# Kernel tuning notes

Hardware: AMD Instinct MI355X
Metric: run time of the kernel (lower is better)

## Reference

```python
import jax, jax.numpy as jnp
import numpy as np

K = 1024
H = 16
HID = 4 * K
EPS = 1e-5


def _layernorm(x, g, b):
    mu = jnp.mean(x, axis=-1, keepdims=True)
    var = jnp.var(x, axis=-1, keepdims=True)
    return (x - mu) * jax.lax.rsqrt(var + EPS) * g + b


def _attention(xq, xkv, wq, wk, wv, wo, bo, causal):
    b, t, e = xq.shape
    tc = xkv.shape[1]
    h, s = H, e // H
    scale = e ** (-0.25)  # applied to both q and k, as in the original
    q = (xq @ wq).reshape(b, t, h, s) * scale
    k = (xkv @ wk).reshape(b, tc, h, s) * scale
    v = (xkv @ wv).reshape(b, tc, h, s)
    dot = jnp.einsum('bqhs,bkhs->bhqk', q, k)  # (b,h,t,tc)
    if causal:
        mask = jnp.tril(jnp.ones((t, tc), dtype=bool))
        dot = jnp.where(mask, dot, jnp.finfo(dot.dtype).min)
    att = jax.nn.softmax(dot, axis=-1)
    out = jnp.einsum('bhqk,bkhs->bqhs', att, v).reshape(b, t, e)
    return out @ wo + bo


def setup_inputs() -> dict:
    key = jax.random.key(0)
    ks = jax.random.split(key, 16)
    sd = K ** -0.5
    inp = {
        'x': jax.random.normal(ks[0], (4, 1024, K), jnp.float32),
        'context': jax.random.normal(ks[1], (4, 1024, K), jnp.float32),
        'sa_wq': jax.random.normal(ks[2], (K, K), jnp.float32) * sd,
        'sa_wk': jax.random.normal(ks[3], (K, K), jnp.float32) * sd,
        'sa_wv': jax.random.normal(ks[4], (K, K), jnp.float32) * sd,
        'sa_wo': jax.random.normal(ks[5], (K, K), jnp.float32) * sd,
        'sa_bo': jnp.zeros((K,), jnp.float32),
        'ca_wq': jax.random.normal(ks[6], (K, K), jnp.float32) * sd,
        'ca_wk': jax.random.normal(ks[7], (K, K), jnp.float32) * sd,
        'ca_wv': jax.random.normal(ks[8], (K, K), jnp.float32) * sd,
        'ca_wo': jax.random.normal(ks[9], (K, K), jnp.float32) * sd,
        'ca_bo': jnp.zeros((K,), jnp.float32),
        'n1_g': jnp.ones((K,), jnp.float32), 'n1_b': jnp.zeros((K,), jnp.float32),
        'n2_g': jnp.ones((K,), jnp.float32), 'n2_b': jnp.zeros((K,), jnp.float32),
        'n3_g': jnp.ones((K,), jnp.float32), 'n3_b': jnp.zeros((K,), jnp.float32),
        'ff_w1': jax.random.normal(ks[10], (K, HID), jnp.float32) * sd,
        'ff_b1': jnp.zeros((HID,), jnp.float32),
        'ff_w2': jax.random.normal(ks[11], (HID, K), jnp.float32) * (HID ** -0.5),
        'ff_b2': jnp.zeros((K,), jnp.float32),
    }
    return inp


def reference(x, context, sa_wq, sa_wk, sa_wv, sa_wo, sa_bo,
              ca_wq, ca_wk, ca_wv, ca_wo, ca_bo,
              n1_g, n1_b, n2_g, n2_b, n3_g, n3_b,
              ff_w1, ff_b1, ff_w2, ff_b2):
    # Masked self-attention + residual + LN (dropout is identity in eval mode)
    sa = _attention(x, x, sa_wq, sa_wk, sa_wv, sa_wo, sa_bo, causal=True)
    x = _layernorm(x + sa, n1_g, n1_b)
    # Cross-attention + residual + LN
    ca = _attention(x, context, ca_wq, ca_wk, ca_wv, ca_wo, ca_bo, causal=False)
    x = _layernorm(x + ca, n2_g, n2_b)
    # FFN + residual + LN
    ff = jax.nn.relu(x @ ff_w1 + ff_b1) @ ff_w2 + ff_b2
    x = _layernorm(x + ff, n3_g, n3_b)
    return x
```

## Files before the change

### kernel.cpp

```cpp
#include <hip/hip_runtime.h>

typedef __bf16 bf16x8 __attribute__((ext_vector_type(8)));
typedef __bf16 bf16x4 __attribute__((ext_vector_type(4)));
typedef float floatx4 __attribute__((ext_vector_type(4)));

#define EMB 1024
#define MROWS 4096
#define HIDN 4096
#define PSTRIDE ((size_t)MROWS * EMB)

__device__ __forceinline__ void load_lds16(const __bf16* g, __bf16* l) {
    __builtin_amdgcn_global_load_lds(
        (const __attribute__((address_space(1))) void*)g,
        (__attribute__((address_space(3))) void*)l, 16, 0, 0);
}

__global__ void transpose_cast_kernel(const float* __restrict__ in,
                                      __bf16* __restrict__ out, int R, int C) {
    __shared__ float tile[32][33];
    int tx = threadIdx.x, ty = threadIdx.y;
    int c0 = blockIdx.x * 32, r0 = blockIdx.y * 32;
#pragma unroll
    for (int i = 0; i < 32; i += 8)
        tile[ty + i][tx] = in[(size_t)(r0 + ty + i) * C + c0 + tx];
    __syncthreads();
#pragma unroll
    for (int i = 0; i < 32; i += 8)
        out[(size_t)(c0 + ty + i) * R + r0 + tx] = (__bf16)tile[tx][ty + i];
}

struct TC8 { const float* s[8]; __bf16* d[8]; };
__global__ void transpose_cast8_kernel(TC8 a) {
    __shared__ float tile[32][33];
    const float* in = a.s[blockIdx.z];
    __bf16* out = a.d[blockIdx.z];
    int tx = threadIdx.x, ty = threadIdx.y;
    int c0 = blockIdx.x * 32, r0 = blockIdx.y * 32;
#pragma unroll
    for (int i = 0; i < 32; i += 8)
        tile[ty + i][tx] = in[(size_t)(r0 + ty + i) * EMB + c0 + tx];
    __syncthreads();
#pragma unroll
    for (int i = 0; i < 32; i += 8)
        out[(size_t)(c0 + ty + i) * EMB + r0 + tx] = (__bf16)tile[tx][ty + i];
}

__global__ void transpose_v_kernel(const __bf16* __restrict__ in,
                                   __bf16* __restrict__ vt, int ld, int Tc) {
    __shared__ __bf16 tile[32][33];
    int tx = threadIdx.x, ty = threadIdx.y;
    int t0 = blockIdx.x * 32, s0 = blockIdx.y * 32;
    int bh = blockIdx.z, b = bh >> 4, h = bh & 15;
#pragma unroll
    for (int i = 0; i < 32; i += 8)
        tile[ty + i][tx] = in[(size_t)(b * Tc + t0 + ty + i) * ld + h * 64 + s0 + tx];
    __syncthreads();
#pragma unroll
    for (int i = 0; i < 32; i += 8)
        vt[((size_t)bh * 64 + s0 + ty + i) * Tc + t0 + tx] = tile[tx][ty + i];
}

__global__ void cast_bf16_kernel(const float* __restrict__ in,
                                 __bf16* __restrict__ out, int n) {
    int i = (blockIdx.x * 256 + threadIdx.x) * 4;
    if (i >= n) return;
    float4 v = *(const float4*)(in + i);
    bf16x4 o;
    o[0] = (__bf16)v.x; o[1] = (__bf16)v.y; o[2] = (__bf16)v.z; o[3] = (__bf16)v.w;
    *(bf16x4*)(out + i) = o;
}

template <int RELU>
__launch_bounds__(256, 4)
__global__ void gemm_bt(const __bf16* __restrict__ A, const __bf16* __restrict__ Bt,
                        __bf16* __restrict__ cb, __bf16* __restrict__ cbalt,
                        const float* __restrict__ bias,
                        int M, int N, int Kd, float scale0, float scale1,
                        int split, int fx, int fy) {
    __shared__ alignas(16) __bf16 As[128 * 32];
    __shared__ alignas(16) __bf16 Bs[128 * 32];
    int tid  = threadIdx.x;
    int wv   = tid >> 6, lane = tid & 63;

    int L   = blockIdx.x + gridDim.x * (blockIdx.y + gridDim.y * blockIdx.z);
    int xcd = L & 7, j = L >> 3;
    int ff  = fx * fy;
    int zw  = xcd / ff;
    int rr  = xcd % ff;
    int nxf = gridDim.x / fx;
    int bnw = (j % nxf) * fx + (rr % fx);
    int bmw = (j / nxf) * fy + (rr / fx);
    int bn  = bnw * 128, bm = bmw * 128;

    int wm   = (wv & 1) * 64, wn = (wv >> 1) * 64;
    int l16  = lane & 15, g16 = lane >> 4;

    int kc   = Kd / gridDim.z;
    int zoff = zw * kc;

    const __bf16* ag0 = A  + (size_t)(bm + (tid >> 2)) * Kd + zoff + (tid & 3) * 8;
    const __bf16* ag1 = ag0 + (size_t)64 * Kd;
    const __bf16* bg0 = Bt + (size_t)(bn + (tid >> 2)) * Kd + zoff + (tid & 3) * 8;
    const __bf16* bg1 = bg0 + (size_t)64 * Kd;
    __bf16* al0 = &As[tid * 8];
    __bf16* al1 = &As[2048 + tid * 8];
    __bf16* bl0 = &Bs[tid * 8];
    __bf16* bl1 = &Bs[2048 + tid * 8];

    floatx4 acc[4][4] = {};

    for (int k0 = 0; k0 < kc; k0 += 32) {
        __syncthreads();
        load_lds16(ag0, al0); load_lds16(ag1, al1);
        load_lds16(bg0, bl0); load_lds16(bg1, bl1);
        ag0 += 32; ag1 += 32; bg0 += 32; bg1 += 32;
        __syncthreads();
        bf16x8 af[4], bfr[4];
#pragma unroll
        for (int i = 0; i < 4; ++i)
            af[i] = *(const bf16x8*)&As[(wm + i * 16 + l16) * 32 + g16 * 8];
#pragma unroll
        for (int jj = 0; jj < 4; ++jj)
            bfr[jj] = *(const bf16x8*)&Bs[(wn + jj * 16 + l16) * 32 + g16 * 8];
#pragma unroll
        for (int i = 0; i < 4; ++i)
#pragma unroll
            for (int jj = 0; jj < 4; ++jj)
                acc[i][jj] = __builtin_amdgcn_mfma_f32_16x16x32_bf16(af[i], bfr[jj], acc[i][jj], 0, 0, 0);
    }

    __bf16* Cp = (zw == 0) ? cb : cbalt + (size_t)(zw - 1) * M * N;
    const float* bz = (zw == 0) ? bias : nullptr;

#pragma unroll
    for (int jj = 0; jj < 4; ++jj) {
        int col  = bn + wn + jj * 16 + l16;
        float sc = (col < split) ? scale0 : scale1;
        float bv = bz ? bz[col] : 0.f;
#pragma unroll
        for (int i = 0; i < 4; ++i) {
            int row0 = bm + wm + i * 16 + g16 * 4;
#pragma unroll
            for (int r = 0; r < 4; ++r) {
                float v = acc[i][jj][r] * sc + bv;
                if (RELU) v = fmaxf(v, 0.f);
                Cp[(size_t)(row0 + r) * N + col] = (__bf16)v;
            }
        }
    }
}

__launch_bounds__(256, 4)
__global__ void attn_kernel(const __bf16* __restrict__ qb, const __bf16* __restrict__ q2,
                            const __bf16* __restrict__ kb, const __bf16* __restrict__ vt,
                            int ldq, int ldk,
                            __bf16* __restrict__ out, int causal, int Tc) {
    constexpr int T = 1024;
    __shared__ alignas(16) __bf16 Qs[64 * 72];
    __shared__ alignas(16) __bf16 Ks[64 * 72];
    __shared__ alignas(16) __bf16 Vs[64 * 72];
    __shared__ alignas(16) __bf16 Ps[4][16 * 72];

    int tid = threadIdx.x;
    int wv = tid >> 6, lane = tid & 63;
    int qt = (blockIdx.x + 4 * blockIdx.z) & 15;
    int h = blockIdx.y, b = blockIdx.z;
    int l16 = lane & 15, g16 = lane >> 4;

#pragma unroll
    for (int cc = 0; cc < 2; ++cc) {
        int c = tid + cc * 256;
        int r = c >> 3, s8 = (c & 7) * 8;
        size_t go = (size_t)(b * T + qt * 64 + r) * ldq + h * 64 + s8;
        bf16x8 qv = *(const bf16x8*)(qb + go);
        if (q2) {
            bf16x8 q2v = *(const bf16x8*)(q2 + go);
#pragma unroll
            for (int e = 0; e < 8; ++e) qv[e] = (__bf16)((float)qv[e] + (float)q2v[e]);
        }
        *(bf16x8*)&Qs[r * 72 + s8] = qv;
    }

    floatx4 oacc[4] = {};
    float mi = -1e30f, li = 0.f;

    int ktmax = causal ? (qt + 1) : (Tc / 64);
    for (int kt = 0; kt < ktmax; ++kt) {
        __syncthreads();
#pragma unroll
        for (int cc = 0; cc < 2; ++cc) {
            int c = tid + cc * 256;
            int r = c >> 3, s8 = (c & 7) * 8;
            bf16x8 kv8 = *(const bf16x8*)(kb + (size_t)(b * Tc + kt * 64 + r) * ldk + h * 64 + s8);
            *(bf16x8*)&Ks[r * 72 + s8] = kv8;
            bf16x8 vv8 = *(const bf16x8*)(vt + ((size_t)(b * 16 + h) * 64 + r) * Tc + kt * 64 + s8);
            *(bf16x8*)&Vs[r * 72 + s8] = vv8;
        }
        __syncthreads();

        floatx4 sacc[4] = {};
#pragma unroll
        for (int kk = 0; kk < 2; ++kk) {
            bf16x8 bq = *(const bf16x8*)&Qs[(wv * 16 + l16) * 72 + kk * 32 + g16 * 8];
#pragma unroll
            for (int j = 0; j < 4; ++j) {
                bf16x8 ak = *(const bf16x8*)&Ks[(j * 16 + l16) * 72 + kk * 32 + g16 * 8];
                sacc[j] = __builtin_amdgcn_mfma_f32_16x16x32_bf16(ak, bq, sacc[j], 0, 0, 0);
            }
        }
        if (causal && kt == qt) {
            int qloc = wv * 16 + l16;
#pragma unroll
            for (int j = 0; j < 4; ++j)
#pragma unroll
                for (int r = 0; r < 4; ++r)
                    if (j * 16 + g16 * 4 + r > qloc) sacc[j][r] = -1e30f;
        }

        float mt = -1e30f;
#pragma unroll
        for (int j = 0; j < 4; ++j)
#pragma unroll
            for (int r = 0; r < 4; ++r) mt = fmaxf(mt, sacc[j][r]);
        mt = fmaxf(mt, __shfl_xor(mt, 16));
        mt = fmaxf(mt, __shfl_xor(mt, 32));
        float mnew  = fmaxf(mi, mt);
        float alpha = __expf(mi - mnew);
        mi = mnew;
        float ls = 0.f;
#pragma unroll
        for (int j = 0; j < 4; ++j) {
            bf16x4 pk;
#pragma unroll
            for (int r = 0; r < 4; ++r) {
                float p = __expf(sacc[j][r] - mnew);
                ls += p;
                pk[r] = (__bf16)p;
            }
            *(bf16x4*)&Ps[wv][l16 * 72 + j * 16 + g16 * 4] = pk;
        }
        ls += __shfl_xor(ls, 16);
        ls += __shfl_xor(ls, 32);
        li = li * alpha + ls;
#pragma unroll
        for (int j = 0; j < 4; ++j) {
            oacc[j][0] *= alpha; oacc[j][1] *= alpha;
            oacc[j][2] *= alpha; oacc[j][3] *= alpha;
        }
#pragma unroll
        for (int kk = 0; kk < 2; ++kk) {
            bf16x8 bp = *(const bf16x8*)&Ps[wv][l16 * 72 + kk * 32 + g16 * 8];
#pragma unroll
            for (int j = 0; j < 4; ++j) {
                bf16x8 av = *(const bf16x8*)&Vs[(j * 16 + l16) * 72 + kk * 32 + g16 * 8];
                oacc[j] = __builtin_amdgcn_mfma_f32_16x16x32_bf16(av, bp, oacc[j], 0, 0, 0);
            }
        }
    }

    __syncthreads();
    float inv = 1.f / li;
#pragma unroll
    for (int j = 0; j < 4; ++j) {
        bf16x4 ok;
#pragma unroll
        for (int r = 0; r < 4; ++r) ok[r] = (__bf16)(oacc[j][r] * inv);
        *(bf16x4*)&Ks[(wv * 16 + l16) * 72 + j * 16 + g16 * 4] = ok;
    }
    int rr = lane >> 2, c4 = (lane & 3) * 16;
    bf16x8 o0 = *(const bf16x8*)&Ks[(wv * 16 + rr) * 72 + c4];
    bf16x8 o1 = *(const bf16x8*)&Ks[(wv * 16 + rr) * 72 + c4 + 8];
    size_t ob = (size_t)(b * T + qt * 64 + wv * 16 + rr) * EMB + h * 64 + c4;
    *(bf16x8*)&out[ob]     = o0;
    *(bf16x8*)&out[ob + 8] = o1;
}

__launch_bounds__(256)
__global__ void ln_kernel(const float* __restrict__ res,
                          const __bf16* __restrict__ pb, int np,
                          const float* __restrict__ g, const float* __restrict__ be,
                          float* __restrict__ outf, __bf16* __restrict__ outb) {
    __shared__ float red[8];
    int row = blockIdx.x, tid = threadIdx.x;
    size_t base = (size_t)row * EMB;
    float4 v = ((const float4*)(res + base))[tid];
    for (int i = 0; i < np; ++i) {
        bf16x4 u = *(const bf16x4*)(pb + i * PSTRIDE + base + tid * 4);
        v.x += (float)u[0]; v.y += (float)u[1];
        v.z += (float)u[2]; v.w += (float)u[3];
    }
    float s  = v.x + v.y + v.z + v.w;
    float ss = v.x * v.x + v.y * v.y + v.z * v.z + v.w * v.w;
#pragma unroll
    for (int o = 1; o < 64; o <<= 1) { s += __shfl_xor(s, o); ss += __shfl_xor(ss, o); }
    if ((tid & 63) == 0) { red[(tid >> 6) * 2] = s; red[(tid >> 6) * 2 + 1] = ss; }
    __syncthreads();
    s  = red[0] + red[2] + red[4] + red[6];
    ss = red[1] + red[3] + red[5] + red[7];
    float mu  = s * (1.0f / 1024.0f);
    float var = ss * (1.0f / 1024.0f) - mu * mu;
    float rs  = rsqrtf(var + 1e-5f);
    float4 gg = ((const float4*)g)[tid];
    float4 bb = ((const float4*)be)[tid];
    float4 y;
    y.x = (v.x - mu) * rs * gg.x + bb.x;
    y.y = (v.y - mu) * rs * gg.y + bb.y;
    y.z = (v.z - mu) * rs * gg.z + bb.z;
    y.w = (v.w - mu) * rs * gg.w + bb.w;
    ((float4*)(outf + base))[tid] = y;
    if (outb) {
        bf16x4 o;
        o[0] = (__bf16)y.x; o[1] = (__bf16)y.y; o[2] = (__bf16)y.z; o[3] = (__bf16)y.w;
        *(bf16x4*)(outb + base + tid * 4) = o;
    }
}

extern "C" void kernel_launch(void* const* d_in, const int* in_sizes, int n_in,
                              void* d_out, int out_size, void* d_ws, size_t ws_size,
                              hipStream_t stream) {
    const float* x     = (const float*)d_in[0];
    const float* ctx   = (const float*)d_in[1];
    const float* sa_wq = (const float*)d_in[2];
    const float* sa_wk = (const float*)d_in[3];
    const float* sa_wv = (const float*)d_in[4];
    const float* sa_wo = (const float*)d_in[5];
    const float* sa_bo = (const float*)d_in[6];
    const float* ca_wq = (const float*)d_in[7];
    const float* ca_wk = (const float*)d_in[8];
    const float* ca_wv = (const float*)d_in[9];
    const float* ca_wo = (const float*)d_in[10];
    const float* ca_bo = (const float*)d_in[11];
    const float* n1_g = (const float*)d_in[12];
    const float* n1_b = (const float*)d_in[13];
    const float* n2_g = (const float*)d_in[14];
    const float* n2_b = (const float*)d_in[15];
    const float* n3_g = (const float*)d_in[16];
    const float* n3_b = (const float*)d_in[17];
    const float* ff_w1 = (const float*)d_in[18];
    const float* ff_b1 = (const float*)d_in[19];
    const float* ff_w2 = (const float*)d_in[20];
    const float* ff_b2 = (const float*)d_in[21];

    size_t off = 0;
    auto alloc = [&](size_t bytes) {
        void* p = (char*)d_ws + off;
        off += (bytes + 255) & ~(size_t)255;
        return p;
    };
    __bf16* w_sa_qkvT = (__bf16*)alloc((size_t)3 * EMB * EMB * 2);
    __bf16* w_sa_oT   = (__bf16*)alloc((size_t)EMB * EMB * 2);
    __bf16* w_ca_qT   = (__bf16*)alloc((size_t)EMB * EMB * 2);
    __bf16* w_ca_kvT  = (__bf16*)alloc((size_t)2 * EMB * EMB * 2);
    __bf16* w_ca_oT   = (__bf16*)alloc((size_t)EMB * EMB * 2);
    __bf16* w1T       = (__bf16*)alloc((size_t)HIDN * EMB * 2);
    __bf16* w2T       = (__bf16*)alloc((size_t)EMB * HIDN * 2);
    __bf16* xb        = (__bf16*)alloc((size_t)MROWS * EMB * 2);
    __bf16* qkv       = (__bf16*)alloc((size_t)MROWS * 3 * EMB * 2);
    __bf16* ao        = (__bf16*)alloc((size_t)MROWS * EMB * 2);
    __bf16* hid       = (__bf16*)alloc((size_t)MROWS * HIDN * 2);
    __bf16* x1b       = (__bf16*)alloc((size_t)MROWS * EMB * 2);
    __bf16* vt        = (__bf16*)alloc((size_t)MROWS * EMB * 2);
    float* res1       = (float*)alloc((size_t)MROWS * EMB * 4);
    float* res2       = (float*)alloc((size_t)MROWS * EMB * 4);

    __bf16* qx0 = qkv;
    __bf16* qx1 = hid;
    __bf16* kvc = qkv + PSTRIDE;
    __bf16* pbo = qkv;
    __bf16* pbf = xb;

    const float s4 = 0.17677669529663687f;
    dim3 tb(32, 8);

    TC8 tc;
    tc.s[0] = sa_wq; tc.d[0] = w_sa_qkvT;
    tc.s[1] = sa_wk; tc.d[1] = w_sa_qkvT + (size_t)EMB * EMB;
    tc.s[2] = sa_wv; tc.d[2] = w_sa_qkvT + (size_t)2 * EMB * EMB;
    tc.s[3] = sa_wo; tc.d[3] = w_sa_oT;
    tc.s[4] = ca_wq; tc.d[4] = w_ca_qT;
    tc.s[5] = ca_wk; tc.d[5] = w_ca_kvT;
    tc.s[6] = ca_wv; tc.d[6] = w_ca_kvT + (size_t)EMB * EMB;
    tc.s[7] = ca_wo; tc.d[7] = w_ca_oT;
    transpose_cast8_kernel<<<dim3(32, 32, 8), tb, 0, stream>>>(tc);
    transpose_cast_kernel<<<dim3(128, 32), tb, 0, stream>>>(ff_w1, w1T, EMB, HIDN);
    transpose_cast_kernel<<<dim3(32, 128), tb, 0, stream>>>(ff_w2, w2T, HIDN, EMB);

    cast_bf16_kernel<<<4096, 256, 0, stream>>>(x, xb, MROWS * EMB);
    gemm_bt<0><<<dim3(24, 32), 256, 0, stream>>>(xb, w_sa_qkvT, qkv, nullptr, nullptr,
        MROWS, 3 * EMB, EMB, s4, 1.f, 2048, 2, 4);
    transpose_v_kernel<<<dim3(32, 2, 64), tb, 0, stream>>>(qkv + 2 * EMB, vt, 3 * EMB, 1024);
    attn_kernel<<<dim3(16, 16, 4), 256, 0, stream>>>(qkv, nullptr, qkv + EMB, vt,
                                                     3 * EMB, 3 * EMB, ao, 1, 1024);
    gemm_bt<0><<<dim3(8, 32, 2), 256, 0, stream>>>(ao, w_sa_oT, pbo, pbo + PSTRIDE, sa_bo,
        MROWS, EMB, EMB, 1.f, 1.f, 0, 2, 2);
    ln_kernel<<<4096, 256, 0, stream>>>(x, pbo, 2, n1_g, n1_b, res1, x1b);

    cast_bf16_kernel<<<4096, 256, 0, stream>>>(ctx, xb, MROWS * EMB);
    gemm_bt<0><<<dim3(16, 32), 256, 0, stream>>>(xb, w_ca_kvT, kvc, nullptr, nullptr,
        MROWS, 2 * EMB, EMB, s4, 1.f, 1024, 2, 4);
    gemm_bt<0><<<dim3(8, 32, 2), 256, 0, stream>>>(x1b, w_ca_qT, qx0, qx1, nullptr,
        MROWS, EMB, EMB, s4, s4, 1 << 30, 2, 2);
    transpose_v_kernel<<<dim3(32, 2, 64), tb, 0, stream>>>(kvc + EMB, vt, 2 * EMB, 1024);
    attn_kernel<<<dim3(16, 16, 4), 256, 0, stream>>>(qx0, qx1, kvc, vt,
                                                     EMB, 2 * EMB, ao, 0, 1024);
    gemm_bt<0><<<dim3(8, 32, 2), 256, 0, stream>>>(ao, w_ca_oT, pbo, pbo + PSTRIDE, ca_bo,
        MROWS, EMB, EMB, 1.f, 1.f, 0, 2, 2);
    ln_kernel<<<4096, 256, 0, stream>>>(res1, pbo, 2, n2_g, n2_b, res2, x1b);

    gemm_bt<1><<<dim3(32, 32), 256, 0, stream>>>(x1b, w1T, hid, nullptr, ff_b1,
        MROWS, HIDN, EMB, 1.f, 1.f, 0, 2, 4);
    gemm_bt<0><<<dim3(8, 32, 4), 256, 0, stream>>>(hid, w2T, pbf, pbf + PSTRIDE, ff_b2,
        MROWS, EMB, HIDN, 1.f, 1.f, 0, 1, 2);
    ln_kernel<<<4096, 256, 0, stream>>>(res2, pbf, 4, n3_g, n3_b, (float*)d_out, nullptr);
}
```

Before: 489.7 us.

## Prefetch K/V tiles in registers, remap attention blocks per XCD, fold softmax scale into Q

The attention kernel now issues the global loads for the next K/V tile into registers while the current tile is being computed, so load latency overlaps with the MFMA work. The grid becomes 1D, and blocks are remapped so that each (batch, head) pair stays on one XCD, with query tiles in bit-reversed order to balance the causal work. The 1/sqrt(d) and log2(e) factors are folded into the Q projection scale, which lets the kernel use the exp2 intrinsic, and K is no longer scaled. The costs are higher register pressure, which can hurt occupancy, and a dependence on a specific block-to-XCD dispatch assumption.

```diff
diff --git a/kernel.cpp b/kernel.cpp
--- a/kernel.cpp
+++ b/kernel.cpp
@@ -163,38 +163,63 @@
 
     int tid = threadIdx.x;
     int wv = tid >> 6, lane = tid & 63;
-    int qt = (blockIdx.x + 4 * blockIdx.z) & 15;
-    int h = blockIdx.y, b = blockIdx.z;
     int l16 = lane & 15, g16 = lane >> 4;
 
-#pragma unroll
-    for (int cc = 0; cc < 2; ++cc) {
-        int c = tid + cc * 256;
-        int r = c >> 3, s8 = (c & 7) * 8;
-        size_t go = (size_t)(b * T + qt * 64 + r) * ldq + h * 64 + s8;
-        bf16x8 qv = *(const bf16x8*)(qb + go);
+    int L = blockIdx.x;
+    int xcd = L & 7, idx = L >> 3;
+    int i4 = idx & 15;
+    int qt = ((i4 & 1) << 3) | ((i4 & 2) << 1) | ((i4 & 4) >> 1) | ((i4 & 8) >> 3);
+    int pair = xcd + 8 * (idx >> 4);
+    int h = pair & 15, b = pair >> 4;
+
+    int r0 = tid >> 3, s8 = (tid & 7) * 8;
+    int r1 = r0 + 32;
+
+    {
+        size_t go0 = (size_t)(b * T + qt * 64 + r0) * ldq + h * 64 + s8;
+        size_t go1 = (size_t)(b * T + qt * 64 + r1) * ldq + h * 64 + s8;
+        bf16x8 qv0 = *(const bf16x8*)(qb + go0);
+        bf16x8 qv1 = *(const bf16x8*)(qb + go1);
         if (q2) {
-            bf16x8 q2v = *(const bf16x8*)(q2 + go);
-#pragma unroll
-            for (int e = 0; e < 8; ++e) qv[e] = (__bf16)((float)qv[e] + (float)q2v[e]);
-        }
-        *(bf16x8*)&Qs[r * 72 + s8] = qv;
+            bf16x8 a0 = *(const bf16x8*)(q2 + go0);
+            bf16x8 a1 = *(const bf16x8*)(q2 + go1);
+#pragma unroll
+            for (int e = 0; e < 8; ++e) {
+                qv0[e] = (__bf16)((float)qv0[e] + (float)a0[e]);
+                qv1[e] = (__bf16)((float)qv1[e] + (float)a1[e]);
+            }
+        }
+        *(bf16x8*)&Qs[r0 * 72 + s8] = qv0;
+        *(bf16x8*)&Qs[r1 * 72 + s8] = qv1;
     }
 
     floatx4 oacc[4] = {};
     float mi = -1e30f, li = 0.f;
 
     int ktmax = causal ? (qt + 1) : (Tc / 64);
+
+    const __bf16* kbase = kb + (size_t)b * Tc * ldk + h * 64 + s8;
+    const __bf16* vbase = vt + (size_t)(b * 16 + h) * 64 * Tc + s8;
+
+    bf16x8 kc0 = *(const bf16x8*)(kbase + (size_t)r0 * ldk);
+    bf16x8 kc1 = *(const bf16x8*)(kbase + (size_t)r1 * ldk);
+    bf16x8 vc0 = *(const bf16x8*)(vbase + (size_t)r0 * Tc);
+    bf16x8 vc1 = *(const bf16x8*)(vbase + (size_t)r1 * Tc);
+    bf16x8 kn0, kn1, vn0, vn1;
+
     for (int kt = 0; kt < ktmax; ++kt) {
         __syncthreads();
-#pragma unroll
-        for (int cc = 0; cc < 2; ++cc) {
-            int c = tid + cc * 256;
-            int r = c >> 3, s8 = (c & 7) * 8;
-            bf16x8 kv8 = *(const bf16x8*)(kb + (size_t)(b * Tc + kt * 64 + r) * ldk + h * 64 + s8);
-            *(bf16x8*)&Ks[r * 72 + s8] = kv8;
-            bf16x8 vv8 = *(const bf16x8*)(vt + ((size_t)(b * 16 + h) * 64 + r) * Tc + kt * 64 + s8);
-            *(bf16x8*)&Vs[r * 72 + s8] = vv8;
+        *(bf16x8*)&Ks[r0 * 72 + s8] = kc0;
+        *(bf16x8*)&Ks[r1 * 72 + s8] = kc1;
+        *(bf16x8*)&Vs[r0 * 72 + s8] = vc0;
+        *(bf16x8*)&Vs[r1 * 72 + s8] = vc1;
+        if (kt + 1 < ktmax) {
+            const __bf16* kp = kbase + (size_t)(kt + 1) * 64 * ldk;
+            const __bf16* vp = vbase + (size_t)(kt + 1) * 64;
+            kn0 = *(const bf16x8*)(kp + (size_t)r0 * ldk);
+            kn1 = *(const bf16x8*)(kp + (size_t)r1 * ldk);
+            vn0 = *(const bf16x8*)(vp + (size_t)r0 * Tc);
+            vn1 = *(const bf16x8*)(vp + (size_t)r1 * Tc);
         }
         __syncthreads();
 
@@ -225,7 +250,7 @@
         mt = fmaxf(mt, __shfl_xor(mt, 16));
         mt = fmaxf(mt, __shfl_xor(mt, 32));
         float mnew  = fmaxf(mi, mt);
-        float alpha = __expf(mi - mnew);
+        float alpha = __builtin_amdgcn_exp2f(mi - mnew);
         mi = mnew;
         float ls = 0.f;
 #pragma unroll
@@ -233,7 +258,7 @@
             bf16x4 pk;
 #pragma unroll
             for (int r = 0; r < 4; ++r) {
-                float p = __expf(sacc[j][r] - mnew);
+                float p = __builtin_amdgcn_exp2f(sacc[j][r] - mnew);
                 ls += p;
                 pk[r] = (__bf16)p;
             }
@@ -256,6 +281,7 @@
                 oacc[j] = __builtin_amdgcn_mfma_f32_16x16x32_bf16(av, bp, oacc[j], 0, 0, 0);
             }
         }
+        kc0 = kn0; kc1 = kn1; vc0 = vn0; vc1 = vn1;
     }
 
     __syncthreads();
@@ -267,10 +293,10 @@
         for (int r = 0; r < 4; ++r) ok[r] = (__bf16)(oacc[j][r] * inv);
         *(bf16x4*)&Ks[(wv * 16 + l16) * 72 + j * 16 + g16 * 4] = ok;
     }
-    int rr = lane >> 2, c4 = (lane & 3) * 16;
-    bf16x8 o0 = *(const bf16x8*)&Ks[(wv * 16 + rr) * 72 + c4];
-    bf16x8 o1 = *(const bf16x8*)&Ks[(wv * 16 + rr) * 72 + c4 + 8];
-    size_t ob = (size_t)(b * T + qt * 64 + wv * 16 + rr) * EMB + h * 64 + c4;
+    int rw = lane >> 2, c4 = (lane & 3) * 16;
+    bf16x8 o0 = *(const bf16x8*)&Ks[(wv * 16 + rw) * 72 + c4];
+    bf16x8 o1 = *(const bf16x8*)&Ks[(wv * 16 + rw) * 72 + c4 + 8];
+    size_t ob = (size_t)(b * T + qt * 64 + wv * 16 + rw) * EMB + h * 64 + c4;
     *(bf16x8*)&out[ob]     = o0;
     *(bf16x8*)&out[ob + 8] = o1;
 }
@@ -369,7 +395,7 @@
     __bf16* pbo = qkv;
     __bf16* pbf = xb;
 
-    const float s4 = 0.17677669529663687f;
+    const float QSC = 0.04508422002778011f;
     dim3 tb(32, 8);
 
     TC8 tc;
@@ -387,22 +413,22 @@
 
     cast_bf16_kernel<<<4096, 256, 0, stream>>>(x, xb, MROWS * EMB);
     gemm_bt<0><<<dim3(24, 32), 256, 0, stream>>>(xb, w_sa_qkvT, qkv, nullptr, nullptr,
-        MROWS, 3 * EMB, EMB, s4, 1.f, 2048, 2, 4);
+        MROWS, 3 * EMB, EMB, QSC, 1.f, 1024, 2, 4);
     transpose_v_kernel<<<dim3(32, 2, 64), tb, 0, stream>>>(qkv + 2 * EMB, vt, 3 * EMB, 1024);
-    attn_kernel<<<dim3(16, 16, 4), 256, 0, stream>>>(qkv, nullptr, qkv + EMB, vt,
-                                                     3 * EMB, 3 * EMB, ao, 1, 1024);
+    attn_kernel<<<1024, 256, 0, stream>>>(qkv, nullptr, qkv + EMB, vt,
+                                          3 * EMB, 3 * EMB, ao, 1, 1024);
     gemm_bt<0><<<dim3(8, 32, 2), 256, 0, stream>>>(ao, w_sa_oT, pbo, pbo + PSTRIDE, sa_bo,
         MROWS, EMB, EMB, 1.f, 1.f, 0, 2, 2);
     ln_kernel<<<4096, 256, 0, stream>>>(x, pbo, 2, n1_g, n1_b, res1, x1b);
 
     cast_bf16_kernel<<<4096, 256, 0, stream>>>(ctx, xb, MROWS * EMB);
     gemm_bt<0><<<dim3(16, 32), 256, 0, stream>>>(xb, w_ca_kvT, kvc, nullptr, nullptr,
-        MROWS, 2 * EMB, EMB, s4, 1.f, 1024, 2, 4);
+        MROWS, 2 * EMB, EMB, 1.f, 1.f, 0, 2, 4);
     gemm_bt<0><<<dim3(8, 32, 2), 256, 0, stream>>>(x1b, w_ca_qT, qx0, qx1, nullptr,
-        MROWS, EMB, EMB, s4, s4, 1 << 30, 2, 2);
+        MROWS, EMB, EMB, QSC, QSC, 1 << 30, 2, 2);
     transpose_v_kernel<<<dim3(32, 2, 64), tb, 0, stream>>>(kvc + EMB, vt, 2 * EMB, 1024);
-    attn_kernel<<<dim3(16, 16, 4), 256, 0, stream>>>(qx0, qx1, kvc, vt,
-                                                     EMB, 2 * EMB, ao, 0, 1024);
+    attn_kernel<<<1024, 256, 0, stream>>>(qx0, qx1, kvc, vt,
+                                          EMB, 2 * EMB, ao, 0, 1024);
     gemm_bt<0><<<dim3(8, 32, 2), 256, 0, stream>>>(ao, w_ca_oT, pbo, pbo + PSTRIDE, ca_bo,
         MROWS, EMB, EMB, 1.f, 1.f, 0, 2, 2);
     ln_kernel<<<4096, 256, 0, stream>>>(res1, pbo, 2, n2_g, n2_b, res2, x1b);
```

New measurement: 495.5 us. No clear change (+1.2%).
